# Kernel optimization log

Hardware: AMD Instinct MI355X
Metric: run time of the kernel (lower is better)

## Reference

```python
import jax, jax.numpy as jnp
import numpy as np

B, L, C, D, H = 32, 4096, 64, 512, 720
EPS = 1e-5

def _xavier(key, shape):
    fan_in, fan_out = shape
    lim = float(np.sqrt(6.0 / (fan_in + fan_out)))
    return jax.random.uniform(key, shape, minval=-lim, maxval=lim, dtype=jnp.float32)

def setup_inputs() -> dict:
    key = jax.random.key(0)
    ks = jax.random.split(key, 8)
    return {
        "x": jax.random.normal(ks[0], (B, L, C), dtype=jnp.float32),
        "alpha": jnp.full((C,), 0.5, dtype=jnp.float32),
        "rev_w": jnp.ones((C,), dtype=jnp.float32),
        "rev_b": jnp.zeros((C,), dtype=jnp.float32),
        "se_w": _xavier(ks[1], (C, D)), "se_b": jnp.zeros((D,), jnp.float32),
        "sp_w": _xavier(ks[2], (D, C)), "sp_b": jnp.zeros((C,), jnp.float32),
        "st_w": _xavier(ks[3], (L, H)), "st_b": jnp.zeros((H,), jnp.float32),
        "te_w": _xavier(ks[4], (C, D)), "te_b": jnp.zeros((D,), jnp.float32),
        "tp_w": _xavier(ks[5], (D, C)), "tp_b": jnp.zeros((C,), jnp.float32),
        "tt_w": _xavier(ks[6], (L, H)), "tt_b": jnp.zeros((H,), jnp.float32),
    }

def _path(z, ew, eb, pw, pb, tw, tb):
    # z: (B,L,C) -> embed C->D -> (identity backbone) -> proj D->C -> temporal L->H
    h = z @ ew + eb            # (B,L,D)
    h = h @ pw + pb            # (B,L,C)
    h = jnp.einsum('blc,lh->bhc', h, tw) + tb[None, :, None]  # (B,H,C)
    return h

def reference(x, alpha, rev_w, rev_b, se_w, se_b, sp_w, sp_b, st_w, st_b,
              te_w, te_b, tp_w, tp_b, tt_w, tt_b):
    # RevIN norm (stats detached, var unbiased=False)
    mean = jax.lax.stop_gradient(jnp.mean(x, axis=1, keepdims=True))          # (B,1,C)
    stdev = jax.lax.stop_gradient(jnp.sqrt(jnp.var(x, axis=1, keepdims=True) + EPS))
    xn = (x - mean) / stdev * rev_w + rev_b
    # EMA decomposition: trend[t] = a*trend[t-1] + (1-a)*x[t], trend[0]=x[0]
    a = jax.nn.sigmoid(alpha)  # (C,)
    def step(carry, xt):
        nxt = a * carry + (1.0 - a) * xt
        return nxt, nxt
    t0 = xn[:, 0]                                    # (B,C)
    _, tr = jax.lax.scan(step, t0, jnp.swapaxes(xn, 0, 1)[1:])  # (L-1,B,C)
    trend = jnp.swapaxes(jnp.concatenate([t0[None], tr], axis=0), 0, 1)  # (B,L,C)
    seasonal = xn - trend
    out = _path(seasonal, se_w, se_b, sp_w, sp_b, st_w, st_b) \
        + _path(trend,    te_w, te_b, tp_w, tp_b, tt_w, tt_b)   # (B,H,C)
    # RevIN denorm
    out = (out - rev_b) / (rev_w + EPS)
    out = out * stdev + mean
    return out
```

## Files before the change

### kernel.cpp

```cpp
#include <hip/hip_runtime.h>
#include <hip/hip_bf16.h>
#include <string.h>
#include <stdint.h>

typedef __hip_bfloat16 bf16_t;
typedef float f32x4 __attribute__((ext_vector_type(4)));
typedef short bf16x8 __attribute__((ext_vector_type(8)));

#define AS_GLOBAL __attribute__((address_space(1)))
#define AS_LDS    __attribute__((address_space(3)))

static constexpr int Bn = 32, Ln = 4096, Cn = 64, Hn = 720, HPn = 768;
static constexpr float EPSf = 1e-5f;

static constexpr size_t OSR_SLICE = (size_t)Bn * Hn * Cn;

__device__ __forceinline__ short f2bf(float f) {
  bf16_t h = __float2bfloat16(f);
  unsigned short u; memcpy(&u, &h, 2);
  return (short)u;
}

__device__ __forceinline__ float sigm(float v) { return 1.f / (1.f + expf(-v)); }

__global__ void __launch_bounds__(256) k_prep(const float* __restrict__ se_w, const float* __restrict__ sp_w,
                                              const float* __restrict__ se_b, const float* __restrict__ sp_b,
                                              const float* __restrict__ te_w, const float* __restrict__ tp_w,
                                              const float* __restrict__ te_b, const float* __restrict__ tp_b,
                                              float* __restrict__ M, float* __restrict__ cvec) {
  int p = blockIdx.y, dc = blockIdx.x, t = threadIdx.x;
  const float* ew = p ? te_w : se_w;
  const float* pw = p ? tp_w : sp_w;
  const float* eb = p ? te_b : se_b;
  const float* pb = p ? tp_b : sp_b;
  int d0 = dc * 64;
  __shared__ float ews[64][68];
  __shared__ float pws[64][68];
  __shared__ float ebs[64];
#pragma unroll
  for (int q = 0; q < 4; ++q) {
    int fi = t * 4 + q;
    int r = fi >> 4, dd = (fi * 4) & 63;
    *reinterpret_cast<f32x4*>(&ews[r][dd]) = *reinterpret_cast<const f32x4*>(&ew[r * 512 + d0 + dd]);
    int pdd = fi >> 4, c = (fi * 4) & 63;
    *reinterpret_cast<f32x4*>(&pws[pdd][c]) = *reinterpret_cast<const f32x4*>(&pw[(d0 + pdd) * 64 + c]);
  }
  if (t < 64) ebs[t] = eb[d0 + t];
  __syncthreads();
  int r0 = (t >> 4) * 4, c0 = (t & 15) * 4;
  float acc[4][4];
#pragma unroll
  for (int i = 0; i < 4; ++i)
#pragma unroll
    for (int j = 0; j < 4; ++j) acc[i][j] = 0.f;
#pragma unroll 4
  for (int g = 0; g < 16; ++g) {
    int dd = g * 4;
    f32x4 av[4], bv[4];
#pragma unroll
    for (int i = 0; i < 4; ++i) av[i] = *reinterpret_cast<const f32x4*>(&ews[r0 + i][dd]);
#pragma unroll
    for (int d = 0; d < 4; ++d) bv[d] = *reinterpret_cast<const f32x4*>(&pws[dd + d][c0]);
#pragma unroll
    for (int d = 0; d < 4; ++d)
#pragma unroll
      for (int i = 0; i < 4; ++i)
#pragma unroll
        for (int j = 0; j < 4; ++j) acc[i][j] = fmaf(av[i][d], bv[d][j], acc[i][j]);
  }
#pragma unroll
  for (int i = 0; i < 4; ++i)
#pragma unroll
    for (int j = 0; j < 4; ++j)
      atomicAdd(&M[p * 4096 + (r0 + i) * 64 + c0 + j], acc[i][j]);
  if (t < 64) {
    float s = (dc == 0) ? pb[t] : 0.f;
#pragma unroll 8
    for (int dd = 0; dd < 64; ++dd) s = fmaf(ebs[dd], pws[dd][t], s);
    atomicAdd(&cvec[p * 64 + t], s);
  }
}

__global__ void k_wprep(const float* __restrict__ st_w, const float* __restrict__ tt_w,
                        bf16_t* __restrict__ Wt, float* __restrict__ S) {
  int p = blockIdx.z;
  const float* W = p ? tt_w : st_w;
  int l0 = blockIdx.x * 64, h0 = blockIdx.y * 64;
  __shared__ float tile[64][65];
  int row = threadIdx.x >> 6, col = threadIdx.x & 63;
  int h = h0 + col;
  float partial = 0.f;
  for (int r = row; r < 64; r += 4) {
    float v = (h < Hn) ? W[(size_t)(l0 + r) * Hn + h] : 0.f;
    tile[r][col] = v;
    partial += v;
  }
  if (h < Hn) atomicAdd(&S[p * 768 + h], partial);
  __syncthreads();
  short* AF = (short*)Wt + (size_t)p * HPn * Ln;
#pragma unroll
  for (int u = 0; u < 2; ++u) {
    int uid = u * 256 + threadIdx.x;
    int ln = uid & 63, ktl = (uid >> 6) & 1, htl = uid >> 7;
    int fr = ln & 15, hi = ln >> 4;
    int ll = ktl * 32 + hi * 8;
    int hh = htl * 16 + fr;
    bf16x8 v;
#pragma unroll
    for (int e = 0; e < 8; ++e) v[e] = f2bf(tile[ll + e][hh]);
    size_t ht = (size_t)(h0 >> 4) + htl, ktg = (size_t)(l0 >> 5) + ktl;
    *reinterpret_cast<bf16x8*>(&AF[((ht * 128 + ktg) << 9) + ((size_t)ln << 3)]) = v;
  }
}

__global__ void __launch_bounds__(256) k_scanA(const float* __restrict__ x, const float* __restrict__ alpha,
                                               float* __restrict__ Psub, float* __restrict__ Pseg,
                                               float* __restrict__ Ssum, float* __restrict__ Ssq) {
  int b = blockIdx.x, q = threadIdx.y, s = blockIdx.y * 4 + q, t = threadIdx.x;
  int c4 = (t & 15) * 4, sub = t >> 4;
  float a[4], k1[4];
#pragma unroll
  for (int i = 0; i < 4; ++i) { a[i] = sigm(alpha[c4 + i]); k1[i] = 1.f - a[i]; }
  const float* xb = x + ((size_t)b * Ln + s * 64 + sub * 16) * Cn + c4;
  float pr[4] = {0.f, 0.f, 0.f, 0.f}, sm[4] = {0.f, 0.f, 0.f, 0.f}, sq[4] = {0.f, 0.f, 0.f, 0.f};
#pragma unroll
  for (int j = 0; j < 16; ++j) {
    f32x4 v = *reinterpret_cast<const f32x4*>(xb + (size_t)j * Cn);
#pragma unroll
    for (int i = 0; i < 4; ++i) {
      sm[i] += v[i];
      sq[i] = fmaf(v[i], v[i], sq[i]);
      pr[i] = fmaf(a[i], pr[i], k1[i] * v[i]);
    }
  }
  *reinterpret_cast<f32x4*>(&Psub[(((size_t)b * 64 + s) * 4 + sub) * 64 + c4]) =
      (f32x4){pr[0], pr[1], pr[2], pr[3]};
  __shared__ float lp[4][4][64], ls[4][4][64], lq[4][4][64];
#pragma unroll
  for (int i = 0; i < 4; ++i) { lp[q][sub][c4 + i] = pr[i]; ls[q][sub][c4 + i] = sm[i]; lq[q][sub][c4 + i] = sq[i]; }
  __syncthreads();
  int c = t;
  float av = sigm(alpha[c]);
  float a16 = av * av; a16 *= a16; a16 *= a16; a16 *= a16;
  float P = ((lp[q][0][c] * a16 + lp[q][1][c]) * a16 + lp[q][2][c]) * a16 + lp[q][3][c];
  int idx = (b * 64 + s) * 64 + c;
  Pseg[idx] = P;
  Ssum[idx] = ls[q][0][c] + ls[q][1][c] + ls[q][2][c] + ls[q][3][c];
  Ssq[idx]  = lq[q][0][c] + lq[q][1][c] + lq[q][2][c] + lq[q][3][c];
}

__global__ void __launch_bounds__(64) k_scanB(const float* __restrict__ x, const float* __restrict__ alpha,
                                              const float* __restrict__ rev_w, const float* __restrict__ rev_b,
                                              const float* __restrict__ Pseg, const float* __restrict__ Ssum,
                                              const float* __restrict__ Ssq,
                                              float* __restrict__ mean, float* __restrict__ rstd,
                                              float* __restrict__ stdv, float* __restrict__ CarryIn) {
  int b = blockIdx.x, c = threadIdx.x;
  float sm = 0.f, sq = 0.f;
#pragma unroll 8
  for (int s = 0; s < 64; ++s) {
    int idx = (b * 64 + s) * 64 + c;
    sm += Ssum[idx]; sq += Ssq[idx];
  }
  float mn = sm * (1.f / 4096.f);
  float var = sq * (1.f / 4096.f) - mn * mn;
  float sd = sqrtf(var + EPSf);
  float rs = 1.f / sd;
  mean[b * 64 + c] = mn; stdv[b * 64 + c] = sd; rstd[b * 64 + c] = rs;

  float w = rev_w[c], rb = rev_b[c];
  float g = rs * w, d = rb - mn * g;
  float a = sigm(alpha[c]);
  float a2 = a * a, a4 = a2 * a2, a8 = a4 * a4, a16 = a8 * a8, a32 = a16 * a16;
  float a64 = a32 * a32;
  float dk1s = d * (1.f - a64);
  float carry = fmaf(g, x[((size_t)b * Ln) * Cn + c], d);
  for (int so = 0; so < 8; ++so) {
    float pv[8];
#pragma unroll
    for (int i = 0; i < 8; ++i)
      pv[i] = Pseg[((size_t)(b * 64 + so * 8 + i)) * 64 + c];
#pragma unroll
    for (int i = 0; i < 8; ++i) {
      CarryIn[((size_t)(b * 64 + so * 8 + i)) * 64 + c] = carry;
      carry = fmaf(a64, carry, fmaf(g, pv[i], dk1s));
    }
  }
}

__global__ void __launch_bounds__(256) k_scanC(const float* __restrict__ x, const float* __restrict__ alpha,
                                               const float* __restrict__ rev_w, const float* __restrict__ rev_b,
                                               const float* __restrict__ mean, const float* __restrict__ rstd,
                                               const float* __restrict__ CarryIn, const float* __restrict__ Psub,
                                               bf16_t* __restrict__ Zt) {
  int b = blockIdx.x, s = blockIdx.y * 4 + threadIdx.y, t = threadIdx.x;
  int c4 = (t & 15) * 4, sub = t >> 4;
  float g[4], d[4], a[4], k1[4], a16[4], dk[4], tr[4];
#pragma unroll
  for (int i = 0; i < 4; ++i) {
    int c = c4 + i;
    float rs = rstd[b * 64 + c];
    g[i] = rs * rev_w[c]; d[i] = rev_b[c] - mean[b * 64 + c] * g[i];
    a[i] = sigm(alpha[c]); k1[i] = 1.f - a[i];
    float v = a[i] * a[i]; v *= v; v *= v; v *= v;
    a16[i] = v;
    dk[i] = d[i] * (1.f - v);
  }
  f32x4 cs = *reinterpret_cast<const f32x4*>(&CarryIn[((size_t)b * 64 + s) * 64 + c4]);
#pragma unroll
  for (int i = 0; i < 4; ++i) tr[i] = cs[i];
  for (int k = 0; k < sub; ++k) {
    f32x4 p = *reinterpret_cast<const f32x4*>(&Psub[(((size_t)b * 64 + s) * 4 + k) * 64 + c4]);
#pragma unroll
    for (int i = 0; i < 4; ++i) tr[i] = fmaf(a16[i], tr[i], fmaf(g[i], p[i], dk[i]));
  }
  const float* xb = x + ((size_t)b * Ln + s * 64 + sub * 16) * Cn + c4;
  bf16x8 vs[4][2], vt[4][2];
#pragma unroll
  for (int j = 0; j < 16; ++j) {
    f32x4 v = *reinterpret_cast<const f32x4*>(xb + (size_t)j * Cn);
#pragma unroll
    for (int i = 0; i < 4; ++i) {
      float xn = fmaf(g[i], v[i], d[i]);
      tr[i] = fmaf(a[i], tr[i], k1[i] * xn);
      vs[i][j >> 3][j & 7] = f2bf(xn - tr[i]);
      vt[i][j >> 3][j & 7] = f2bf(tr[i]);
    }
  }
#pragma unroll
  for (int i = 0; i < 4; ++i) {
    int c = c4 + i;
    bf16_t* zs = Zt + ((size_t)b * 64 + c) * Ln + s * 64 + sub * 16;
    bf16_t* zt = zs + (size_t)Bn * Cn * Ln;
    *reinterpret_cast<bf16x8*>(zs) = vs[i][0];
    *reinterpret_cast<bf16x8*>(zs + 8) = vs[i][1];
    *reinterpret_cast<bf16x8*>(zt) = vt[i][0];
    *reinterpret_cast<bf16x8*>(zt + 8) = vt[i][1];
  }
}

__device__ __forceinline__ void gload16(const bf16_t* g, bf16_t* l) {
  __builtin_amdgcn_global_load_lds((const AS_GLOBAL uint32_t*)g, (AS_LDS uint32_t*)l, 16, 0, 0);
}

template <int KS>
__global__ void __launch_bounds__(256, 3) k_gemm(const bf16_t* __restrict__ Wt, const bf16_t* __restrict__ Zt,
                                                 float* __restrict__ Osr) {
  int z = blockIdx.z;
  int p = z / KS, kq = z % KS;
  const short* AF = (const short*)Wt + (size_t)p * HPn * Ln;
  const bf16_t* Bz = Zt + (size_t)p * (Bn * Cn) * Ln;
  int h0 = blockIdx.y * 128, n0 = blockIdx.x * 128;
  int kbase = kq * (Ln / KS);
  const int NT = (Ln / KS) / 32;
  __shared__ __align__(16) bf16_t Bl[3][128 * 32];
  int tid = threadIdx.x, wid = tid >> 6, lane = tid & 63;
  int wr = wid >> 1, wc = wid & 1;
  int fr = lane & 15, hi = lane >> 4;
  int kc = (tid & 3) ^ ((tid >> 3) & 3);
  const bf16_t* bbase = Bz + (size_t)(n0 + (tid >> 2)) * Ln + kbase + kc * 8;
  const short* abase = AF + ((((size_t)(h0 >> 4) + wr * 4) * 128 + (kbase >> 5)) << 9) + ((size_t)lane << 3);

  f32x4 acc[4][4];
#pragma unroll
  for (int i = 0; i < 4; ++i)
#pragma unroll
    for (int j = 0; j < 4; ++j) acc[i][j] = (f32x4){0.f, 0.f, 0.f, 0.f};

  auto STAGE_B = [&](int bufi, int kt) {
    gload16(bbase + (size_t)kt * 32, &Bl[bufi][tid * 8]);
    gload16(bbase + (size_t)64 * Ln + kt * 32, &Bl[bufi][2048 + tid * 8]);
  };
  auto ALOAD = [&](bf16x8 (&dst)[4], int kt) {
#pragma unroll
    for (int i = 0; i < 4; ++i)
      dst[i] = *reinterpret_cast<const bf16x8*>(abase + (((size_t)i * 128 + kt) << 9));
  };

  int sw8 = (hi ^ ((fr >> 1) & 3)) * 8;
  auto COMPUTE = [&](int bufi, const bf16x8 (&af)[4]) {
    bf16x8 bfr[4];
#pragma unroll
    for (int j = 0; j < 4; ++j)
      bfr[j] = *reinterpret_cast<const bf16x8*>(&Bl[bufi][(wc * 64 + j * 16 + fr) * 32 + sw8]);
    __builtin_amdgcn_s_setprio(1);
#pragma unroll
    for (int i = 0; i < 4; ++i)
#pragma unroll
      for (int j = 0; j < 4; ++j)
        acc[i][j] = __builtin_amdgcn_mfma_f32_16x16x32_bf16(af[i], bfr[j], acc[i][j], 0, 0, 0);
    __builtin_amdgcn_s_setprio(0);
  };

  bf16x8 aA[4], aB[4];
  STAGE_B(0, 0);
  STAGE_B(1, 1);
  ALOAD(aA, 0);

  auto ITER = [&](int t, int cur, int nx, const bf16x8 (&acur)[4], bf16x8 (&anxt)[4]) {
    __builtin_amdgcn_sched_barrier(0);
    if (t + 1 < NT) { asm volatile("s_waitcnt vmcnt(6)" ::: "memory"); }
    else            { asm volatile("s_waitcnt vmcnt(4)" ::: "memory"); }
    __builtin_amdgcn_s_barrier();
    __builtin_amdgcn_sched_barrier(0);
    if (t + 2 < NT) STAGE_B(nx, t + 2);
    if (t + 1 < NT) ALOAD(anxt, t + 1);
    COMPUTE(cur, acur);
  };

  int cur = 0;
  for (int t = 0; t < NT; t += 2) {
    int c1 = (cur == 2) ? 0 : cur + 1;
    int nx0 = (c1 == 2) ? 0 : c1 + 1;
    int nx1 = cur;
    ITER(t,     cur, nx0, aA, aB);
    ITER(t + 1, c1,  nx1, aB, aA);
    cur = nx0;
  }

#pragma unroll
  for (int i = 0; i < 4; ++i) {
#pragma unroll
    for (int j = 0; j < 4; ++j) {
#pragma unroll
      for (int r = 0; r < 4; ++r) {
        int m = wr * 64 + i * 16 + hi * 4 + r;
        int h = h0 + m;
        if (h < Hn) {
          int n = n0 + wc * 64 + j * 16 + fr;
          int bidx = n >> 6, c = n & 63;
          Osr[(((size_t)z * Bn + bidx) * Hn + h) * Cn + c] = acc[i][j][r];
        }
      }
    }
  }
}

template <int KS>
__global__ void __launch_bounds__(256) k_epi(const float* __restrict__ Osr, const float* __restrict__ M,
                                             const float* __restrict__ cvec, const float* __restrict__ S,
                                             const float* __restrict__ st_b, const float* __restrict__ tt_b,
                                             const float* __restrict__ rev_w, const float* __restrict__ rev_b,
                                             const float* __restrict__ mean, const float* __restrict__ stdv,
                                             float* __restrict__ out) {
  __shared__ float Msh[2][64][64];
  __shared__ float rowS[4][64];
  __shared__ float rowT[4][64];
  int t = threadIdx.x;
  for (int i = t; i < 8192; i += 256) ((float*)Msh)[i] = M[i];
  int g = t >> 6, c = t & 63;
  float w = rev_w[c], rb = rev_b[c];
  float cs = cvec[c], ct = cvec[64 + c];
  int base = blockIdx.x * 16;
  for (int it = 0; it < 4; ++it) {
    int r = base + it * 4 + g;
    int b = r / 720, h = r % 720;
    __syncthreads();
    float vs = 0.f, vt = 0.f;
#pragma unroll
    for (int kq = 0; kq < KS; ++kq) {
      vs += Osr[(((size_t)kq * Bn + b) * Hn + h) * Cn + c];
      vt += Osr[(((size_t)(KS + kq) * Bn + b) * Hn + h) * Cn + c];
    }
    rowS[g][c] = vs;
    rowT[g][c] = vt;
    __syncthreads();
    float acc = cs * S[h] + ct * S[768 + h] + st_b[h] + tt_b[h];
    for (int cp = 0; cp < 64; ++cp)
      acc = fmaf(rowS[g][cp], Msh[0][cp][c], fmaf(rowT[g][cp], Msh[1][cp][c], acc));
    float o = (acc - rb) / (w + EPSf) * stdv[b * Cn + c] + mean[b * Cn + c];
    out[(size_t)r * 64 + c] = o;
  }
}

extern "C" void kernel_launch(void* const* d_in, const int* in_sizes, int n_in,
                              void* d_out, int out_size, void* d_ws, size_t ws_size,
                              hipStream_t stream) {
  const float* x     = (const float*)d_in[0];
  const float* alpha = (const float*)d_in[1];
  const float* rev_w = (const float*)d_in[2];
  const float* rev_b = (const float*)d_in[3];
  const float* se_w  = (const float*)d_in[4];
  const float* se_b  = (const float*)d_in[5];
  const float* sp_w  = (const float*)d_in[6];
  const float* sp_b  = (const float*)d_in[7];
  const float* st_w  = (const float*)d_in[8];
  const float* st_b  = (const float*)d_in[9];
  const float* te_w  = (const float*)d_in[10];
  const float* te_b  = (const float*)d_in[11];
  const float* tp_w  = (const float*)d_in[12];
  const float* tp_b  = (const float*)d_in[13];
  const float* tt_w  = (const float*)d_in[14];
  const float* tt_b  = (const float*)d_in[15];
  float* out = (float*)d_out;

  const size_t SZ_WT  = (size_t)2 * HPn * Ln * 2;
  const size_t SZ_ZT  = (size_t)2 * Bn * Cn * Ln * 2;
  const size_t SZ_SEG = (size_t)Bn * 64 * 64 * 4;
  const size_t SZ_M   = 2 * 64 * 64 * 4;
  const size_t SZ_CV  = 2 * 64 * 4;
  const size_t SZ_S   = 2 * 768 * 4;
  const size_t TAIL   = SZ_M + SZ_CV + SZ_S + 3 * (size_t)Bn * Cn * 4;

  const size_t NEED4 = SZ_WT + SZ_ZT + 8 * OSR_SLICE * 4 + TAIL;
  const int KS = (ws_size >= NEED4) ? 4 : 1;
  const size_t SZ_OSR = (size_t)(2 * KS) * OSR_SLICE * 4;

  char* ws = (char*)d_ws;
  bf16_t* Wt   = (bf16_t*)(ws);
  bf16_t* Zt   = (bf16_t*)(ws + SZ_WT);
  float*  Osr  = (float*)(ws + SZ_WT + SZ_ZT);
  float*  Psub  = Osr;
  float*  Pseg  = (float*)((char*)Psub + 4 * SZ_SEG);
  float*  Ssum  = (float*)((char*)Pseg + SZ_SEG);
  float*  Ssq   = (float*)((char*)Ssum + SZ_SEG);
  float*  Carry = (float*)((char*)Ssq + SZ_SEG);
  char* tail = ws + SZ_WT + SZ_ZT + SZ_OSR;
  float* Mbuf = (float*)tail;                 tail += SZ_M;
  float* cvec = (float*)tail;                 tail += SZ_CV;
  float* S    = (float*)tail;                 tail += SZ_S;
  float* mean = (float*)tail;                 tail += (size_t)Bn * Cn * 4;
  float* rstd = (float*)tail;                 tail += (size_t)Bn * Cn * 4;
  float* stdv = (float*)tail;

  hipMemsetAsync(Mbuf, 0, SZ_M + SZ_CV + SZ_S, stream);

  k_prep<<<dim3(8, 2), 256, 0, stream>>>(se_w, sp_w, se_b, sp_b, te_w, tp_w, te_b, tp_b, Mbuf, cvec);
  k_wprep<<<dim3(64, 12, 2), 256, 0, stream>>>(st_w, tt_w, Wt, S);
  k_scanA<<<dim3(32, 16), dim3(64, 4), 0, stream>>>(x, alpha, Psub, Pseg, Ssum, Ssq);
  k_scanB<<<32, 64, 0, stream>>>(x, alpha, rev_w, rev_b, Pseg, Ssum, Ssq, mean, rstd, stdv, Carry);
  k_scanC<<<dim3(32, 16), dim3(64, 4), 0, stream>>>(x, alpha, rev_w, rev_b, mean, rstd, Carry, Psub, Zt);
  if (KS == 4) {
    k_gemm<4><<<dim3(16, 6, 8), 256, 0, stream>>>(Wt, Zt, Osr);
    k_epi<4><<<1440, 256, 0, stream>>>(Osr, Mbuf, cvec, S, st_b, tt_b, rev_w, rev_b, mean, stdv, out);
  } else {
    k_gemm<1><<<dim3(16, 6, 2), 256, 0, stream>>>(Wt, Zt, Osr);
    k_epi<1><<<1440, 256, 0, stream>>>(Osr, Mbuf, cvec, S, st_b, tt_b, rev_w, rev_b, mean, stdv, out);
  }
}
```

Baseline: 115.6 us.

## Swizzle GEMM blocks across XCDs and register-tile epilogue rows

The GEMM launches a flat 1D grid and remaps block IDs so that consecutive tiles sharing the same p/k-split land on the same XCD, with the aim of improving L2 reuse of Wt and Zt. The epilogue now processes 32 rows per block with 8 rows per thread group held in registers. It loads the split-K partials first, then does a single sync and a register-tiled 64x64 mixing loop that reuses each M element across 8 rows. This removes the per-row syncs and the repeated LDS reads of M, at the cost of more registers and more LDS.

```diff
diff --git a/kernel.cpp b/kernel.cpp
--- a/kernel.cpp
+++ b/kernel.cpp
@@ -246,11 +246,14 @@
 template <int KS>
 __global__ void __launch_bounds__(256, 3) k_gemm(const bf16_t* __restrict__ Wt, const bf16_t* __restrict__ Zt,
                                                  float* __restrict__ Osr) {
-  int z = blockIdx.z;
+  int per = gridDim.x >> 3;
+  int swz = (blockIdx.x & 7) * per + (blockIdx.x >> 3);
+  int z = swz / 96, rem = swz % 96;
+  int by = rem >> 4, bx = rem & 15;
   int p = z / KS, kq = z % KS;
   const short* AF = (const short*)Wt + (size_t)p * HPn * Ln;
   const bf16_t* Bz = Zt + (size_t)p * (Bn * Cn) * Ln;
-  int h0 = blockIdx.y * 128, n0 = blockIdx.x * 128;
+  int h0 = by * 128, n0 = bx * 128;
   int kbase = kq * (Ln / KS);
   const int NT = (Ln / KS) / 32;
   __shared__ __align__(16) bf16_t Bl[3][128 * 32];
@@ -344,32 +347,50 @@
                                              const float* __restrict__ mean, const float* __restrict__ stdv,
                                              float* __restrict__ out) {
   __shared__ float Msh[2][64][64];
-  __shared__ float rowS[4][64];
-  __shared__ float rowT[4][64];
+  __shared__ float rowS[32][64];
+  __shared__ float rowT[32][64];
   int t = threadIdx.x;
   for (int i = t; i < 8192; i += 256) ((float*)Msh)[i] = M[i];
-  int g = t >> 6, c = t & 63;
+  int c = t & 63, grp = t >> 6;
   float w = rev_w[c], rb = rev_b[c];
   float cs = cvec[c], ct = cvec[64 + c];
-  int base = blockIdx.x * 16;
-  for (int it = 0; it < 4; ++it) {
-    int r = base + it * 4 + g;
+  int base = blockIdx.x * 32;
+#pragma unroll
+  for (int k = 0; k < 8; ++k) {
+    int rl = grp * 8 + k;
+    int r = base + rl;
     int b = r / 720, h = r % 720;
-    __syncthreads();
     float vs = 0.f, vt = 0.f;
 #pragma unroll
     for (int kq = 0; kq < KS; ++kq) {
       vs += Osr[(((size_t)kq * Bn + b) * Hn + h) * Cn + c];
       vt += Osr[(((size_t)(KS + kq) * Bn + b) * Hn + h) * Cn + c];
     }
-    rowS[g][c] = vs;
-    rowT[g][c] = vt;
-    __syncthreads();
-    float acc = cs * S[h] + ct * S[768 + h] + st_b[h] + tt_b[h];
-    for (int cp = 0; cp < 64; ++cp)
-      acc = fmaf(rowS[g][cp], Msh[0][cp][c], fmaf(rowT[g][cp], Msh[1][cp][c], acc));
-    float o = (acc - rb) / (w + EPSf) * stdv[b * Cn + c] + mean[b * Cn + c];
-    out[(size_t)r * 64 + c] = o;
+    rowS[rl][c] = vs;
+    rowT[rl][c] = vt;
+  }
+  __syncthreads();
+  float acc[8];
+  int hh[8], bb[8];
+#pragma unroll
+  for (int k = 0; k < 8; ++k) {
+    int r = base + grp * 8 + k;
+    bb[k] = r / 720; hh[k] = r % 720;
+    acc[k] = cs * S[hh[k]] + ct * S[768 + hh[k]] + st_b[hh[k]] + tt_b[hh[k]];
+  }
+  int r0 = grp * 8;
+#pragma unroll 4
+  for (int cp = 0; cp < 64; ++cp) {
+    float m0 = Msh[0][cp][c], m1 = Msh[1][cp][c];
+#pragma unroll
+    for (int k = 0; k < 8; ++k)
+      acc[k] = fmaf(rowS[r0 + k][cp], m0, fmaf(rowT[r0 + k][cp], m1, acc[k]));
+  }
+  float winv = 1.f / (w + EPSf);
+#pragma unroll
+  for (int k = 0; k < 8; ++k) {
+    float o = (acc[k] - rb) * winv * stdv[bb[k] * Cn + c] + mean[bb[k] * Cn + c];
+    out[(size_t)(base + r0 + k) * 64 + c] = o;
   }
 }
 
@@ -431,10 +452,10 @@
   k_scanB<<<32, 64, 0, stream>>>(x, alpha, rev_w, rev_b, Pseg, Ssum, Ssq, mean, rstd, stdv, Carry);
   k_scanC<<<dim3(32, 16), dim3(64, 4), 0, stream>>>(x, alpha, rev_w, rev_b, mean, rstd, Carry, Psub, Zt);
   if (KS == 4) {
-    k_gemm<4><<<dim3(16, 6, 8), 256, 0, stream>>>(Wt, Zt, Osr);
-    k_epi<4><<<1440, 256, 0, stream>>>(Osr, Mbuf, cvec, S, st_b, tt_b, rev_w, rev_b, mean, stdv, out);
+    k_gemm<4><<<768, 256, 0, stream>>>(Wt, Zt, Osr);
+    k_epi<4><<<720, 256, 0, stream>>>(Osr, Mbuf, cvec, S, st_b, tt_b, rev_w, rev_b, mean, stdv, out);
   } else {
-    k_gemm<1><<<dim3(16, 6, 2), 256, 0, stream>>>(Wt, Zt, Osr);
-    k_epi<1><<<1440, 256, 0, stream>>>(Osr, Mbuf, cvec, S, st_b, tt_b, rev_w, rev_b, mean, stdv, out);
-  }
-}
+    k_gemm<1><<<192, 256, 0, stream>>>(Wt, Zt, Osr);
+    k_epi<1><<<720, 256, 0, stream>>>(Osr, Mbuf, cvec, S, st_b, tt_b, rev_w, rev_b, mean, stdv, out);
+  }
+}
```

Result: faster. 108.1 us (-6.5%).
